# Optimization experiments

Hardware: AMD Instinct MI355X
Metric: run time of the kernel (lower is better)

The kernel has to match this reference:

```python
import jax, jax.numpy as jnp
import numpy as np

D_CONV = 4
DT_RANK = 32
D_STATE = 16


def setup_inputs() -> dict:
    key = jax.random.key(0)
    ks = jax.random.split(key, 12)
    B, Lt, d_model, d_inner = 2, 512, 512, 1024
    mk = lambda k, shape, scale=0.02: jax.random.normal(k, shape, dtype=jnp.float32) * scale
    inp = {}
    inp['t0'] = jax.random.normal(ks[0], (B, Lt, d_model), dtype=jnp.float32)
    inp['t1'] = jax.random.normal(ks[1], (B, Lt, d_model), dtype=jnp.float32)
    inp['t2'] = jax.random.normal(ks[2], (B, Lt, d_model), dtype=jnp.float32)
    inp['t3'] = jax.random.normal(ks[3], (B, Lt, d_model), dtype=jnp.float32)
    inp['in_proj_w'] = mk(ks[4], (2 * d_inner, d_model))
    inp['conv_w'] = mk(ks[5], (d_inner, 1, D_CONV), 0.2)
    inp['conv_b'] = jnp.zeros((d_inner,), jnp.float32)
    inp['x_proj_w'] = mk(ks[6], (DT_RANK + 2 * D_STATE, d_inner))
    s = DT_RANK ** (-0.5)
    inp['dt_w'] = jax.random.uniform(ks[7], (d_inner, DT_RANK), minval=-s, maxval=s, dtype=jnp.float32)
    dt = jnp.exp(jax.random.uniform(ks[8], (d_inner,), dtype=jnp.float32) * (np.log(0.1) - np.log(0.001)) + np.log(0.001))
    dt = jnp.clip(dt, 1e-4)
    inp['dt_b'] = dt + jnp.log(-jnp.expm1(-dt))
    inp['A_log'] = jnp.log(jnp.tile(jnp.arange(1, D_STATE + 1, dtype=jnp.float32), (d_inner, 1)))
    inp['D_param'] = jnp.ones((d_inner,), jnp.float32)
    inp['out_proj_w'] = mk(ks[9], (d_model, d_inner))
    return inp


def reference(t0, t1, t2, t3, in_proj_w, conv_w, conv_b, x_proj_w, dt_w, dt_b, A_log, D_param, out_proj_w):
    tensors = [t0, t1, t2, t3]
    # interleaved gather/concat: [B, 4*Lt, d_model]
    x = jnp.concatenate([t[:, i::4, :] for i in range(4) for t in tensors], axis=1)
    L = x.shape[1]
    xz = x @ in_proj_w.T                      # [B, L, 2*d_inner]
    xc, z = jnp.split(xz, 2, axis=-1)
    # causal depthwise conv1d (torch pads both sides K-1 then truncates to L == left pad only)
    xc = xc.transpose(0, 2, 1)                # [B, d_inner, L]
    xc = jax.lax.conv_general_dilated(
        xc, conv_w, window_strides=(1,), padding=[(D_CONV - 1, 0)],
        dimension_numbers=('NCH', 'OIH', 'NCH'), feature_group_count=xc.shape[1])
    xc = xc + conv_b[None, :, None]
    xc = jax.nn.silu(xc.transpose(0, 2, 1))   # [B, L, d_inner]
    # SSM
    A = -jnp.exp(A_log)                       # [d_inner, d_state]
    dbc = xc @ x_proj_w.T                     # [B, L, dt_rank + 2*d_state]
    delta, Bm, Cm = jnp.split(dbc, [DT_RANK, DT_RANK + D_STATE], axis=-1)
    delta = jax.nn.softplus(delta @ dt_w.T + dt_b)  # [B, L, d_inner]
    deltaA = jnp.exp(delta[..., None] * A)          # [B, L, d_inner, d_state]
    BX = (delta * xc)[..., None] * Bm[:, :, None, :]  # deltaB * x

    def op(c1, c2):
        a1, b1 = c1
        a2, b2 = c2
        return a1 * a2, a2 * b1 + b2

    _, hs = jax.lax.associative_scan(op, (deltaA, BX), axis=1)  # h_t = dA_t h_{t-1} + BX_t
    y = jnp.einsum('blds,bls->bld', hs, Cm) + D_param * xc
    out = (y * jax.nn.silu(z)) @ out_proj_w.T  # [B, L, d_model]
    Lt = L // 4
    return tuple(out[:, i::4, :][:, :Lt, :] + tensors[i] for i in range(4))
```

## Files before the change

kernel.cpp:

```cpp
#include <hip/hip_runtime.h>

#define NB 2
#define LT 512
#define LL 2048
#define MM 4096
#define DMODEL 512
#define DINNER 1024
#define DTRANK 32
#define DSTATE 16
#define NSEG 128
#define SEGLEN 16
#define NST (NB * DINNER * DSTATE)
#define NSCAN (NSEG * NB * DINNER)
#define KCH 8

typedef short bf16x8 __attribute__((ext_vector_type(8)));
typedef float f32x4  __attribute__((ext_vector_type(4)));

__device__ __forceinline__ float silu_f(float x) { return x / (1.f + __expf(-x)); }
__device__ __forceinline__ unsigned short f2b(float f) {
    unsigned u = __float_as_uint(f);
    u += 0x7fffu + ((u >> 16) & 1u);
    return (unsigned short)(u >> 16);
}
__device__ __forceinline__ float b2f(unsigned short u) {
    return __uint_as_float(((unsigned)u) << 16);
}
__device__ __forceinline__ float bhi(unsigned u) {
    return __uint_as_float(u & 0xFFFF0000u);
}
__device__ __forceinline__ float blo(unsigned u) {
    return __uint_as_float(u << 16);
}

__global__ __launch_bounds__(256) void k_prep(
    const float* __restrict__ t0, const float* __restrict__ t1,
    const float* __restrict__ t2, const float* __restrict__ t3,
    const float* __restrict__ Wi, const float* __restrict__ Wx,
    unsigned short* __restrict__ xg_b, unsigned short* __restrict__ wib,
    unsigned short* __restrict__ wxb)
{
    const int blk = blockIdx.x;
    if (blk < 1024) {
        const int idx = blk * 256 + threadIdx.x;
        const int m = idx >> 6;
        const int c8 = (idx & 63) * 8;
        const int b = m >> 11;
        const int l = m & 2047;
        const int c = l >> 7, r = l & 127;
        const int ti = c & 3, ci = c >> 2;
        const float* tp = (ti == 0) ? t0 : (ti == 1) ? t1 : (ti == 2) ? t2 : t3;
        const float* src = tp + ((size_t)b * 512 + (size_t)(ci + 4 * r)) * 512 + c8;
        float4 v0 = *(const float4*)(src + 0);
        float4 v1 = *(const float4*)(src + 4);
        bf16x8 o;
        o[0]=f2b(v0.x); o[1]=f2b(v0.y); o[2]=f2b(v0.z); o[3]=f2b(v0.w);
        o[4]=f2b(v1.x); o[5]=f2b(v1.y); o[6]=f2b(v1.z); o[7]=f2b(v1.w);
        *(bf16x8*)(xg_b + (size_t)m * DMODEL + c8) = o;
    } else if (blk < 2048) {
        const int off = (blk - 1024) * 256 + threadIdx.x;
        float4 v = *(const float4*)(Wi + (size_t)off * 4);
        ushort4 o;
        o.x = f2b(v.x); o.y = f2b(v.y); o.z = f2b(v.z); o.w = f2b(v.w);
        *(ushort4*)(wib + (size_t)off * 4) = o;
    } else {
        const int off = (blk - 2048) * 256 + threadIdx.x;
        float4 v = *(const float4*)(Wx + (size_t)off * 4);
        ushort4 o;
        o.x = f2b(v.x); o.y = f2b(v.y); o.z = f2b(v.z); o.w = f2b(v.w);
        *(ushort4*)(wxb + (size_t)off * 4) = o;
    }
}

__global__ __launch_bounds__(256) void k_inproj(
    const unsigned short* __restrict__ xg_b, const unsigned short* __restrict__ wib,
    float* __restrict__ xc_raw, unsigned short* __restrict__ zb)
{
    __shared__ short As[128 * 40];
    __shared__ short Bs[128 * 40];
    const int t = threadIdx.x;
    const int lane = t & 63;
    const int wid = t >> 6;
    const int wm = wid >> 1, wn = wid & 1;
    const int bm = blockIdx.x, bn = blockIdx.y;

    const int srow  = t >> 1;
    const int shalf = (t & 1) * 16;

    const unsigned short* asrc = xg_b + (size_t)(bm * 128 + srow) * DMODEL + shalf;
    const unsigned short* bsrc = wib + (size_t)(bn * 128 + srow) * DMODEL + shalf;

    f32x4 acc[4][4];
#pragma unroll
    for (int i = 0; i < 4; ++i)
#pragma unroll
        for (int j = 0; j < 4; ++j) acc[i][j] = (f32x4){0.f, 0.f, 0.f, 0.f};

    bf16x8 ra0 = *(const bf16x8*)(asrc + 0);
    bf16x8 ra1 = *(const bf16x8*)(asrc + 8);
    bf16x8 rb0 = *(const bf16x8*)(bsrc + 0);
    bf16x8 rb1 = *(const bf16x8*)(bsrc + 8);

    const int ko = (lane >> 4) * 8;
    const int fr = lane & 15;

    for (int ks = 0; ks < DMODEL / 32; ++ks) {
        __syncthreads();
        *(bf16x8*)&As[srow * 40 + shalf]     = ra0;
        *(bf16x8*)&As[srow * 40 + shalf + 8] = ra1;
        *(bf16x8*)&Bs[srow * 40 + shalf]     = rb0;
        *(bf16x8*)&Bs[srow * 40 + shalf + 8] = rb1;
        __syncthreads();
        if (ks + 1 < DMODEL / 32) {
            const int k0 = (ks + 1) * 32;
            ra0 = *(const bf16x8*)(asrc + k0 + 0);
            ra1 = *(const bf16x8*)(asrc + k0 + 8);
            rb0 = *(const bf16x8*)(bsrc + k0 + 0);
            rb1 = *(const bf16x8*)(bsrc + k0 + 8);
        }
        bf16x8 af[4], bfr[4];
#pragma unroll
        for (int mf = 0; mf < 4; ++mf)
            af[mf] = *(const bf16x8*)&As[(wm * 64 + mf * 16 + fr) * 40 + ko];
#pragma unroll
        for (int nf = 0; nf < 4; ++nf)
            bfr[nf] = *(const bf16x8*)&Bs[(wn * 64 + nf * 16 + fr) * 40 + ko];
#pragma unroll
        for (int mf = 0; mf < 4; ++mf)
#pragma unroll
            for (int nf = 0; nf < 4; ++nf)
                acc[mf][nf] = __builtin_amdgcn_mfma_f32_16x16x32_bf16(
                    af[mf], bfr[nf], acc[mf][nf], 0, 0, 0);
    }

    if (bn < 8) {
#pragma unroll
        for (int mf = 0; mf < 4; ++mf) {
            const int gmb = bm * 128 + wm * 64 + mf * 16 + (lane >> 4) * 4;
#pragma unroll
            for (int nf = 0; nf < 4; ++nf) {
                const int gn = bn * 128 + wn * 64 + nf * 16 + (lane & 15);
#pragma unroll
                for (int j = 0; j < 4; ++j)
                    xc_raw[(size_t)(gmb + j) * DINNER + gn] = acc[mf][nf][j];
            }
        }
    } else {
#pragma unroll
        for (int mf = 0; mf < 4; ++mf) {
            const int gmb = bm * 128 + wm * 64 + mf * 16 + (lane >> 4) * 4;
#pragma unroll
            for (int nf = 0; nf < 4; ++nf) {
                const int gn = bn * 128 + wn * 64 + nf * 16 + (lane & 15) - 1024;
#pragma unroll
                for (int j = 0; j < 4; ++j)
                    zb[(size_t)(gmb + j) * DINNER + gn] = f2b(acc[mf][nf][j]);
            }
        }
    }
}

__global__ __launch_bounds__(256) void k_conv(
    const float* __restrict__ xc_raw, const float* __restrict__ cw,
    const float* __restrict__ cb, const unsigned short* __restrict__ zb,
    unsigned short* __restrict__ xc_b, unsigned int* __restrict__ xzp)
{
    const int d  = blockIdx.y * 256 + threadIdx.x;
    const int mt = blockIdx.x;
    const int m0 = mt * 16;
    const int l0 = m0 & 2047;

    float w[4];
#pragma unroll
    for (int k = 0; k < 4; ++k) w[k] = cw[(size_t)d * 4 + k];
    const float bias = cb[d];

    float r[19];
#pragma unroll
    for (int o = 0; o < 19; ++o) {
        const int l = l0 + o - 3;
        r[o] = (l >= 0) ? xc_raw[(size_t)(m0 + o - 3) * DINNER + d] : 0.f;
    }

#pragma unroll
    for (int mm = 0; mm < 16; ++mm) {
        float s = bias;
#pragma unroll
        for (int k = 0; k < 4; ++k) s += w[k] * r[mm + k];
        const unsigned short x16 = f2b(silu_f(s));
        const size_t idx = (size_t)(m0 + mm) * DINNER + d;
        const unsigned short z16 = zb[idx];
        xc_b[idx] = x16;
        xzp[idx] = ((unsigned)z16 << 16) | (unsigned)x16;
    }
}

__global__ __launch_bounds__(256) void k_xproj_mfma(
    const unsigned short* __restrict__ xc_b, const unsigned short* __restrict__ wxb,
    float* __restrict__ part)
{
    __shared__ short As[128 * 136];
    __shared__ short Bs[64 * 136];
    const int t = threadIdx.x;
    const int lane = t & 63;
    const int w = t >> 6;
    const int bm = blockIdx.x;
    const int kc = blockIdx.y;

    {
        const int row = t >> 1;
        const int cb0 = (t & 1) * 64;
        const unsigned short* src = xc_b + (size_t)(bm * 128 + row) * 1024 + kc * 128 + cb0;
#pragma unroll
        for (int q = 0; q < 8; ++q)
            *(bf16x8*)&As[row * 136 + cb0 + q * 8] = *(const bf16x8*)(src + q * 8);
    }
    {
        const int row = t >> 2;
        const int cb0 = (t & 3) * 32;
        const unsigned short* src = wxb + (size_t)row * 1024 + kc * 128 + cb0;
#pragma unroll
        for (int q = 0; q < 4; ++q)
            *(bf16x8*)&Bs[row * 136 + cb0 + q * 8] = *(const bf16x8*)(src + q * 8);
    }
    __syncthreads();

    const int fr = lane & 15;
    const int ko = (lane >> 4) * 8;

    f32x4 acc[2][4];
#pragma unroll
    for (int i = 0; i < 2; ++i)
#pragma unroll
        for (int j = 0; j < 4; ++j) acc[i][j] = (f32x4){0.f, 0.f, 0.f, 0.f};

#pragma unroll
    for (int ks = 0; ks < 4; ++ks) {
        const int kb = ks * 32 + ko;
        bf16x8 af[2], bfr[4];
#pragma unroll
        for (int mf = 0; mf < 2; ++mf)
            af[mf] = *(const bf16x8*)&As[(w * 32 + mf * 16 + fr) * 136 + kb];
#pragma unroll
        for (int nf = 0; nf < 4; ++nf)
            bfr[nf] = *(const bf16x8*)&Bs[(nf * 16 + fr) * 136 + kb];
#pragma unroll
        for (int mf = 0; mf < 2; ++mf)
#pragma unroll
            for (int nf = 0; nf < 4; ++nf)
                acc[mf][nf] = __builtin_amdgcn_mfma_f32_16x16x32_bf16(
                    af[mf], bfr[nf], acc[mf][nf], 0, 0, 0);
    }

    float* pb = part + (size_t)kc * (MM * 64);
#pragma unroll
    for (int mf = 0; mf < 2; ++mf) {
        const int rb = bm * 128 + w * 32 + mf * 16 + (lane >> 4) * 4;
#pragma unroll
        for (int nf = 0; nf < 4; ++nf) {
            const int col = nf * 16 + (lane & 15);
#pragma unroll
            for (int j = 0; j < 4; ++j)
                pb[(size_t)(rb + j) * 64 + col] = acc[mf][nf][j];
        }
    }
}

__global__ __launch_bounds__(256) void k_xreduce(
    const float* __restrict__ part, float* __restrict__ dbc)
{
    const int i = blockIdx.x * 256 + threadIdx.x;
    float s = 0.f;
#pragma unroll
    for (int kc = 0; kc < KCH; ++kc)
        s += part[(size_t)kc * (MM * 64) + i];
    dbc[i] = s;
}

__global__ __launch_bounds__(256) void k_dtproj(
    const float* __restrict__ dbc, const float* __restrict__ dtw,
    const float* __restrict__ dtb, const unsigned short* __restrict__ xc_b,
    unsigned int* __restrict__ dxp)
{
    const int tid = threadIdx.x;
    const int m0 = blockIdx.x * 16;
    const int d  = blockIdx.y * 256 + tid;

    float w[DTRANK];
#pragma unroll
    for (int q = 0; q < 8; ++q) {
        float4 v = *(const float4*)(dtw + (size_t)d * DTRANK + q * 4);
        w[q * 4 + 0] = v.x; w[q * 4 + 1] = v.y;
        w[q * 4 + 2] = v.z; w[q * 4 + 3] = v.w;
    }
    const float bias = dtb[d];

#pragma unroll 4
    for (int m = 0; m < 16; ++m) {
        const float* bc = dbc + (size_t)(m0 + m) * 64;
        float s0 = bias, s1 = 0.f, s2 = 0.f, s3 = 0.f;
#pragma unroll
        for (int r = 0; r < DTRANK; r += 4) {
            s0 += bc[r + 0] * w[r + 0];
            s1 += bc[r + 1] * w[r + 1];
            s2 += bc[r + 2] * w[r + 2];
            s3 += bc[r + 3] * w[r + 3];
        }
        const float s = (s0 + s1) + (s2 + s3);
        const float sp = (s > 20.f) ? s : __logf(1.f + __expf(s));
        const size_t idx = (size_t)(m0 + m) * DINNER + d;
        const float xv = b2f(xc_b[idx]);
        dxp[idx] = ((unsigned)f2b(sp * xv) << 16) | (unsigned)f2b(sp);
    }
}

__global__ __launch_bounds__(256) void k_scan_partial(
    const unsigned int* __restrict__ dxp, const float* __restrict__ dbc,
    const float* __restrict__ A_log, unsigned int* __restrict__ hab)
{
    __shared__ float Bsh[4][16][16];
    const int gid = blockIdx.x * 256 + threadIdx.x;
    const int d = gid & 1023;
    const int b = (gid >> 10) & (NB - 1);
    const int g = gid >> 11;
    const int w = threadIdx.x >> 6;
    const int lane = threadIdx.x & 63;

    const int mbase = b * LL + g * SEGLEN;

    {
        const int r0 = lane >> 4;
        const int cc = lane & 15;
#pragma unroll
        for (int rq = 0; rq < 4; ++rq) {
            const int row = rq * 4 + r0;
            Bsh[w][row][cc] = dbc[(size_t)(mbase + row) * 64 + 32 + cc];
        }
    }

    float Af[DSTATE];
#pragma unroll
    for (int q = 0; q < 4; ++q) {
        float4 a4 = *(const float4*)(A_log + d * DSTATE + q * 4);
        Af[q * 4 + 0] = -__expf(a4.x);
        Af[q * 4 + 1] = -__expf(a4.y);
        Af[q * 4 + 2] = -__expf(a4.z);
        Af[q * 4 + 3] = -__expf(a4.w);
    }

    unsigned uu[16];
#pragma unroll
    for (int m = 0; m < 16; ++m)
        uu[m] = dxp[(size_t)(mbase + m) * DINNER + d];

    __syncthreads();

    float h[DSTATE], ap[DSTATE];
#pragma unroll
    for (int s = 0; s < DSTATE; ++s) { h[s] = 0.f; ap[s] = 1.f; }

#pragma unroll
    for (int ll = 0; ll < SEGLEN; ++ll) {
        const float de = blo(uu[ll]);
        const float dx = bhi(uu[ll]);
        float Bv[DSTATE];
#pragma unroll
        for (int q = 0; q < 4; ++q)
            *(float4*)&Bv[q * 4] = *(const float4*)&Bsh[w][ll][q * 4];
#pragma unroll
        for (int s = 0; s < DSTATE; ++s) {
            const float dA = __expf(de * Af[s]);
            ap[s] *= dA;
            h[s] = dA * h[s] + dx * Bv[s];
        }
    }

    const size_t base = ((size_t)(b * DINNER + d) * NSEG + g) * 16;
    unsigned ob[16];
#pragma unroll
    for (int s = 0; s < DSTATE; ++s)
        ob[s] = ((unsigned)f2b(h[s]) << 16) | (unsigned)f2b(ap[s]);
#pragma unroll
    for (int q = 0; q < 4; ++q)
        *(uint4*)&hab[base + q * 4] = *(const uint4*)&ob[q * 4];
}

__global__ __launch_bounds__(256) void k_scan_combine(
    const unsigned int* __restrict__ hab, unsigned short* __restrict__ hib)
{
    const int tid = blockIdx.x * 256 + threadIdx.x;
    const int g = tid & 63;
    const size_t bd = (size_t)(tid >> 6);
    const size_t base = (bd * NSEG + 2 * g) * 16;

    unsigned u0[16], u1[16];
#pragma unroll
    for (int q = 0; q < 4; ++q) {
        *(uint4*)&u0[q * 4] = *(const uint4*)&hab[base + q * 4];
        *(uint4*)&u1[q * 4] = *(const uint4*)&hab[base + 16 + q * 4];
    }

    float A0[16], B0[16], A[16], B[16];
#pragma unroll
    for (int s = 0; s < 16; ++s) {
        A0[s] = blo(u0[s]); B0[s] = bhi(u0[s]);
        const float A1 = blo(u1[s]), B1 = bhi(u1[s]);
        A[s] = A1 * A0[s];
        B[s] = A1 * B0[s] + B1;
    }
#pragma unroll
    for (int off = 1; off < 64; off <<= 1) {
#pragma unroll
        for (int s = 0; s < 16; ++s) {
            const float Ap = __shfl_up(A[s], off, 64);
            const float Bp = __shfl_up(B[s], off, 64);
            if (g >= off) { B[s] = A[s] * Bp + B[s]; A[s] = A[s] * Ap; }
        }
    }
    unsigned short E[16], E1[16];
#pragma unroll
    for (int s = 0; s < 16; ++s) {
        float e = __shfl_up(B[s], 1, 64);
        if (g == 0) e = 0.f;
        E[s]  = f2b(e);
        E1[s] = f2b(A0[s] * e + B0[s]);
    }
#pragma unroll
    for (int q = 0; q < 2; ++q) {
        *(bf16x8*)&hib[base + q * 8]      = *(const bf16x8*)&E[q * 8];
        *(bf16x8*)&hib[base + 16 + q * 8] = *(const bf16x8*)&E1[q * 8];
    }
}

__global__ __launch_bounds__(256) void k_scan_final(
    const unsigned int* __restrict__ dxp, const unsigned int* __restrict__ xzp,
    const float* __restrict__ dbc, const float* __restrict__ A_log,
    const float* __restrict__ Dp, const unsigned short* __restrict__ hib,
    unsigned short* __restrict__ yzb)
{
    __shared__ float BC[4][16][32];
    const int gid = blockIdx.x * 256 + threadIdx.x;
    const int d = gid & 1023;
    const int b = (gid >> 10) & (NB - 1);
    const int g = gid >> 11;
    const int w = threadIdx.x >> 6;
    const int lane = threadIdx.x & 63;

    const int mbase = b * LL + g * SEGLEN;

    {
        const int r0 = lane >> 5;
        const int cc = lane & 31;
#pragma unroll
        for (int rq = 0; rq < 8; ++rq) {
            const int row = rq * 2 + r0;
            BC[w][row][cc] = dbc[(size_t)(mbase + row) * 64 + 32 + cc];
        }
    }

    float Af[DSTATE];
#pragma unroll
    for (int q = 0; q < 4; ++q) {
        float4 a4 = *(const float4*)(A_log + d * DSTATE + q * 4);
        Af[q * 4 + 0] = -__expf(a4.x);
        Af[q * 4 + 1] = -__expf(a4.y);
        Af[q * 4 + 2] = -__expf(a4.z);
        Af[q * 4 + 3] = -__expf(a4.w);
    }
    const float Dd = Dp[d];

    unsigned uu[16], vv[16];
#pragma unroll
    for (int m = 0; m < 16; ++m) {
        uu[m] = dxp[(size_t)(mbase + m) * DINNER + d];
        vv[m] = xzp[(size_t)(mbase + m) * DINNER + d];
    }

    float h[DSTATE];
    {
        const size_t base = ((size_t)(b * DINNER + d) * NSEG + g) * 16;
        bf16x8 h0 = *(const bf16x8*)&hib[base];
        bf16x8 h1 = *(const bf16x8*)&hib[base + 8];
#pragma unroll
        for (int s = 0; s < 8; ++s) {
            h[s]     = b2f((unsigned short)h0[s]);
            h[s + 8] = b2f((unsigned short)h1[s]);
        }
    }

    __syncthreads();

#pragma unroll
    for (int ll = 0; ll < SEGLEN; ++ll) {
        const float de = blo(uu[ll]);
        const float dx = bhi(uu[ll]);
        const float x  = blo(vv[ll]);
        const float zz = bhi(vv[ll]);
        float Bv[DSTATE], Cv[DSTATE];
#pragma unroll
        for (int q = 0; q < 4; ++q) {
            *(float4*)&Bv[q * 4] = *(const float4*)&BC[w][ll][q * 4];
            *(float4*)&Cv[q * 4] = *(const float4*)&BC[w][ll][16 + q * 4];
        }
        float y0 = 0.f, y1 = 0.f, y2 = 0.f, y3 = 0.f;
#pragma unroll
        for (int s = 0; s < DSTATE; s += 4) {
            float dA;
            dA = __expf(de * Af[s + 0]); h[s + 0] = dA * h[s + 0] + dx * Bv[s + 0]; y0 += h[s + 0] * Cv[s + 0];
            dA = __expf(de * Af[s + 1]); h[s + 1] = dA * h[s + 1] + dx * Bv[s + 1]; y1 += h[s + 1] * Cv[s + 1];
            dA = __expf(de * Af[s + 2]); h[s + 2] = dA * h[s + 2] + dx * Bv[s + 2]; y2 += h[s + 2] * Cv[s + 2];
            dA = __expf(de * Af[s + 3]); h[s + 3] = dA * h[s + 3] + dx * Bv[s + 3]; y3 += h[s + 3] * Cv[s + 3];
        }
        const float y = (y0 + y1) + (y2 + y3);
        yzb[(size_t)(mbase + ll) * DINNER + d] = f2b((y + Dd * x) * silu_f(zz));
    }
}

__global__ __launch_bounds__(256) void k_outproj(
    const unsigned short* __restrict__ yzb, const float* __restrict__ Wo,
    const float* __restrict__ t0, const float* __restrict__ t1,
    const float* __restrict__ t2, const float* __restrict__ t3,
    float* __restrict__ outp)
{
    __shared__ short As[64 * 40];
    __shared__ short Bs[64 * 40];
    const int t = threadIdx.x;
    const int lane = t & 63;
    const int wid = t >> 6;
    const int wm = wid >> 1, wn = wid & 1;
    const int bm = blockIdx.x;
    const int bn = blockIdx.y;

    const int srow = t >> 2;
    const int scol = (t & 3) * 8;

    const unsigned short* asrc = yzb + (size_t)(bm * 64 + srow) * DINNER + scol;
    const float* bsrc = Wo + (size_t)(bn * 64 + srow) * DINNER + scol;

    f32x4 acc[2][2];
#pragma unroll
    for (int i = 0; i < 2; ++i)
#pragma unroll
        for (int j = 0; j < 2; ++j) acc[i][j] = (f32x4){0.f, 0.f, 0.f, 0.f};

    bf16x8 raA = *(const bf16x8*)asrc;
    float4 rb[2];
#pragma unroll
    for (int q = 0; q < 2; ++q) rb[q] = *(const float4*)(bsrc + q * 4);

    const int ko = (lane >> 4) * 8;
    const int fr = lane & 15;

    for (int ks = 0; ks < DINNER / 32; ++ks) {
        __syncthreads();
        {
            bf16x8 w0;
            w0[0]=f2b(rb[0].x); w0[1]=f2b(rb[0].y); w0[2]=f2b(rb[0].z); w0[3]=f2b(rb[0].w);
            w0[4]=f2b(rb[1].x); w0[5]=f2b(rb[1].y); w0[6]=f2b(rb[1].z); w0[7]=f2b(rb[1].w);
            *(bf16x8*)&As[srow * 40 + scol] = raA;
            *(bf16x8*)&Bs[srow * 40 + scol] = w0;
        }
        __syncthreads();
        if (ks + 1 < DINNER / 32) {
            const int k0 = (ks + 1) * 32;
            raA = *(const bf16x8*)(asrc + k0);
#pragma unroll
            for (int q = 0; q < 2; ++q) rb[q] = *(const float4*)(bsrc + k0 + q * 4);
        }
        bf16x8 af[2], bfr[2];
#pragma unroll
        for (int mf = 0; mf < 2; ++mf)
            af[mf] = *(const bf16x8*)&As[(wm * 32 + mf * 16 + fr) * 40 + ko];
#pragma unroll
        for (int nf = 0; nf < 2; ++nf)
            bfr[nf] = *(const bf16x8*)&Bs[(wn * 32 + nf * 16 + fr) * 40 + ko];
#pragma unroll
        for (int mf = 0; mf < 2; ++mf)
#pragma unroll
            for (int nf = 0; nf < 2; ++nf)
                acc[mf][nf] = __builtin_amdgcn_mfma_f32_16x16x32_bf16(
                    af[mf], bfr[nf], acc[mf][nf], 0, 0, 0);
    }

#pragma unroll
    for (int mf = 0; mf < 2; ++mf) {
#pragma unroll
        for (int j = 0; j < 4; ++j) {
            const int gm = bm * 64 + wm * 32 + mf * 16 + (lane >> 4) * 4 + j;
            const int b = gm >> 11;
            const int l = gm & 2047;
            const int ii = l & 3;
            const int jj = l >> 2;
            const float* tsel = (ii == 0) ? t0 : (ii == 1) ? t1 : (ii == 2) ? t2 : t3;
#pragma unroll
            for (int nf = 0; nf < 2; ++nf) {
                const int gn = bn * 64 + wn * 32 + nf * 16 + (lane & 15);
                const float tv = tsel[((size_t)b * 512 + jj) * 512 + gn];
                outp[(((size_t)ii * NB + b) * 512 + jj) * 512 + gn] = acc[mf][nf][j] + tv;
            }
        }
    }
}

extern "C" void kernel_launch(void* const* d_in, const int* in_sizes, int n_in,
                              void* d_out, int out_size, void* d_ws, size_t ws_size,
                              hipStream_t stream)
{
    const float* t0 = (const float*)d_in[0];
    const float* t1 = (const float*)d_in[1];
    const float* t2 = (const float*)d_in[2];
    const float* t3 = (const float*)d_in[3];
    const float* in_proj_w  = (const float*)d_in[4];
    const float* conv_w     = (const float*)d_in[5];
    const float* conv_b     = (const float*)d_in[6];
    const float* x_proj_w   = (const float*)d_in[7];
    const float* dt_w       = (const float*)d_in[8];
    const float* dt_b       = (const float*)d_in[9];
    const float* A_log      = (const float*)d_in[10];
    const float* D_param    = (const float*)d_in[11];
    const float* out_proj_w = (const float*)d_in[12];
    float* outp = (float*)d_out;

    float* xc_raw = (float*)d_ws;
    unsigned short* xc_b = (unsigned short*)(xc_raw + (size_t)MM * DINNER);
    unsigned int* dxp = (unsigned int*)(xc_b + (size_t)MM * DINNER);
    unsigned int* xzp = dxp + (size_t)MM * DINNER;
    float* dbc  = (float*)(xzp + (size_t)MM * DINNER);
    unsigned int* hab = (unsigned int*)(dbc + (size_t)MM * 64);
    unsigned short* hib = (unsigned short*)(hab + (size_t)NB * DINNER * NSEG * 16);
    float* part  = xc_raw;
    unsigned short* yzb = (unsigned short*)xc_raw;
    unsigned short* zb  = (unsigned short*)hab;
    unsigned short* wxb = hib;
    unsigned short* xg_b = (unsigned short*)dxp;
    unsigned short* wib  = (unsigned short*)xzp;

    k_prep<<<2112, 256, 0, stream>>>(t0, t1, t2, t3, in_proj_w, x_proj_w, xg_b, wib, wxb);
    k_inproj<<<dim3(32, 16), 256, 0, stream>>>(xg_b, wib, xc_raw, zb);
    k_conv<<<dim3(MM / 16, 4), 256, 0, stream>>>(xc_raw, conv_w, conv_b, zb, xc_b, xzp);
    k_xproj_mfma<<<dim3(32, KCH), 256, 0, stream>>>(xc_b, wxb, part);
    k_xreduce<<<(MM * 64) / 256, 256, 0, stream>>>(part, dbc);
    k_dtproj<<<dim3(MM / 16, 4), 256, 0, stream>>>(dbc, dt_w, dt_b, xc_b, dxp);
    k_scan_partial<<<NSCAN / 256, 256, 0, stream>>>(dxp, dbc, A_log, hab);
    k_scan_combine<<<(NB * DINNER * 64) / 256, 256, 0, stream>>>(hab, hib);
    k_scan_final<<<NSCAN / 256, 256, 0, stream>>>(dxp, xzp, dbc, A_log, D_param, hib, yzb);
    k_outproj<<<dim3(64, 8), 256, 0, stream>>>(yzb, out_proj_w, t0, t1, t2, t3, outp);
}
```

Before: 127.6 us.

## Split scan state dimension across four threads per channel

The partial and final scan kernels now assign four threads per (batch, channel, segment), each owning 4 of the 16 SSM states, and launch four times as many threads. In the final scan the per-state output partial sums are combined with two xor shuffles, and only one lane per channel writes. This cuts registers per thread and raises parallelism and occupancy for the latency-bound recurrence. The cost is redundant loads of dxp/xzp per thread, extra shuffles and more blocks.

```diff
diff --git a/kernel.cpp b/kernel.cpp
--- a/kernel.cpp
+++ b/kernel.cpp
@@ -318,34 +318,27 @@
     const unsigned int* __restrict__ dxp, const float* __restrict__ dbc,
     const float* __restrict__ A_log, unsigned int* __restrict__ hab)
 {
-    __shared__ float Bsh[4][16][16];
+    __shared__ float Bsh[16][16];
     const int gid = blockIdx.x * 256 + threadIdx.x;
-    const int d = gid & 1023;
-    const int b = (gid >> 10) & (NB - 1);
-    const int g = gid >> 11;
-    const int w = threadIdx.x >> 6;
-    const int lane = threadIdx.x & 63;
-
+    const int dlocal = gid & 15;
+    const int sg = (gid >> 4) & 3;
+    const int dhi = (gid >> 6) & 63;
+    const int b = (gid >> 12) & (NB - 1);
+    const int g = gid >> 13;
+    const int d = dhi * 16 + dlocal;
     const int mbase = b * LL + g * SEGLEN;
 
     {
-        const int r0 = lane >> 4;
-        const int cc = lane & 15;
-#pragma unroll
-        for (int rq = 0; rq < 4; ++rq) {
-            const int row = rq * 4 + r0;
-            Bsh[w][row][cc] = dbc[(size_t)(mbase + row) * 64 + 32 + cc];
-        }
-    }
-
-    float Af[DSTATE];
-#pragma unroll
-    for (int q = 0; q < 4; ++q) {
-        float4 a4 = *(const float4*)(A_log + d * DSTATE + q * 4);
-        Af[q * 4 + 0] = -__expf(a4.x);
-        Af[q * 4 + 1] = -__expf(a4.y);
-        Af[q * 4 + 2] = -__expf(a4.z);
-        Af[q * 4 + 3] = -__expf(a4.w);
+        const int row = threadIdx.x >> 4;
+        const int cc  = threadIdx.x & 15;
+        Bsh[row][cc] = dbc[(size_t)(mbase + row) * 64 + 32 + cc];
+    }
+
+    float Af[4];
+    {
+        float4 a4 = *(const float4*)(A_log + d * DSTATE + sg * 4);
+        Af[0] = -__expf(a4.x); Af[1] = -__expf(a4.y);
+        Af[2] = -__expf(a4.z); Af[3] = -__expf(a4.w);
     }
 
     unsigned uu[16];
@@ -355,34 +348,27 @@
 
     __syncthreads();
 
-    float h[DSTATE], ap[DSTATE];
-#pragma unroll
-    for (int s = 0; s < DSTATE; ++s) { h[s] = 0.f; ap[s] = 1.f; }
+    float h[4] = {0.f, 0.f, 0.f, 0.f};
+    float ap[4] = {1.f, 1.f, 1.f, 1.f};
 
 #pragma unroll
     for (int ll = 0; ll < SEGLEN; ++ll) {
         const float de = blo(uu[ll]);
         const float dx = bhi(uu[ll]);
-        float Bv[DSTATE];
-#pragma unroll
-        for (int q = 0; q < 4; ++q)
-            *(float4*)&Bv[q * 4] = *(const float4*)&Bsh[w][ll][q * 4];
-#pragma unroll
-        for (int s = 0; s < DSTATE; ++s) {
-            const float dA = __expf(de * Af[s]);
-            ap[s] *= dA;
-            h[s] = dA * h[s] + dx * Bv[s];
-        }
-    }
-
-    const size_t base = ((size_t)(b * DINNER + d) * NSEG + g) * 16;
-    unsigned ob[16];
-#pragma unroll
-    for (int s = 0; s < DSTATE; ++s)
-        ob[s] = ((unsigned)f2b(h[s]) << 16) | (unsigned)f2b(ap[s]);
+        float4 Bv = *(const float4*)&Bsh[ll][sg * 4];
+        float dA;
+        dA = __expf(de * Af[0]); ap[0] *= dA; h[0] = dA * h[0] + dx * Bv.x;
+        dA = __expf(de * Af[1]); ap[1] *= dA; h[1] = dA * h[1] + dx * Bv.y;
+        dA = __expf(de * Af[2]); ap[2] *= dA; h[2] = dA * h[2] + dx * Bv.z;
+        dA = __expf(de * Af[3]); ap[3] *= dA; h[3] = dA * h[3] + dx * Bv.w;
+    }
+
+    const size_t base = ((size_t)(b * DINNER + d) * NSEG + g) * 16 + sg * 4;
+    unsigned ob[4];
 #pragma unroll
     for (int q = 0; q < 4; ++q)
-        *(uint4*)&hab[base + q * 4] = *(const uint4*)&ob[q * 4];
+        ob[q] = ((unsigned)f2b(h[q]) << 16) | (unsigned)f2b(ap[q]);
+    *(uint4*)&hab[base] = *(const uint4*)&ob[0];
 }
 
 __global__ __launch_bounds__(256) void k_scan_combine(
@@ -438,34 +424,30 @@
     const float* __restrict__ Dp, const unsigned short* __restrict__ hib,
     unsigned short* __restrict__ yzb)
 {
-    __shared__ float BC[4][16][32];
+    __shared__ float BC[16][32];
     const int gid = blockIdx.x * 256 + threadIdx.x;
-    const int d = gid & 1023;
-    const int b = (gid >> 10) & (NB - 1);
-    const int g = gid >> 11;
-    const int w = threadIdx.x >> 6;
-    const int lane = threadIdx.x & 63;
-
+    const int dlocal = gid & 15;
+    const int sg = (gid >> 4) & 3;
+    const int dhi = (gid >> 6) & 63;
+    const int b = (gid >> 12) & (NB - 1);
+    const int g = gid >> 13;
+    const int d = dhi * 16 + dlocal;
     const int mbase = b * LL + g * SEGLEN;
 
     {
-        const int r0 = lane >> 5;
-        const int cc = lane & 31;
-#pragma unroll
-        for (int rq = 0; rq < 8; ++rq) {
-            const int row = rq * 2 + r0;
-            BC[w][row][cc] = dbc[(size_t)(mbase + row) * 64 + 32 + cc];
-        }
-    }
-
-    float Af[DSTATE];
-#pragma unroll
-    for (int q = 0; q < 4; ++q) {
-        float4 a4 = *(const float4*)(A_log + d * DSTATE + q * 4);
-        Af[q * 4 + 0] = -__expf(a4.x);
-        Af[q * 4 + 1] = -__expf(a4.y);
-        Af[q * 4 + 2] = -__expf(a4.z);
-        Af[q * 4 + 3] = -__expf(a4.w);
+#pragma unroll
+        for (int q = 0; q < 2; ++q) {
+            const int idx = q * 256 + threadIdx.x;
+            const int row = idx >> 5, cc = idx & 31;
+            BC[row][cc] = dbc[(size_t)(mbase + row) * 64 + 32 + cc];
+        }
+    }
+
+    float Af[4];
+    {
+        float4 a4 = *(const float4*)(A_log + d * DSTATE + sg * 4);
+        Af[0] = -__expf(a4.x); Af[1] = -__expf(a4.y);
+        Af[2] = -__expf(a4.z); Af[3] = -__expf(a4.w);
     }
     const float Dd = Dp[d];
 
@@ -476,16 +458,12 @@
         vv[m] = xzp[(size_t)(mbase + m) * DINNER + d];
     }
 
-    float h[DSTATE];
+    float h[4];
     {
-        const size_t base = ((size_t)(b * DINNER + d) * NSEG + g) * 16;
-        bf16x8 h0 = *(const bf16x8*)&hib[base];
-        bf16x8 h1 = *(const bf16x8*)&hib[base + 8];
-#pragma unroll
-        for (int s = 0; s < 8; ++s) {
-            h[s]     = b2f((unsigned short)h0[s]);
-            h[s + 8] = b2f((unsigned short)h1[s]);
-        }
+        const size_t base = ((size_t)(b * DINNER + d) * NSEG + g) * 16 + sg * 4;
+        ushort4 hv = *(const ushort4*)(hib + base);
+        h[0] = b2f(hv.x); h[1] = b2f(hv.y);
+        h[2] = b2f(hv.z); h[3] = b2f(hv.w);
     }
 
     __syncthreads();
@@ -496,23 +474,18 @@
         const float dx = bhi(uu[ll]);
         const float x  = blo(vv[ll]);
         const float zz = bhi(vv[ll]);
-        float Bv[DSTATE], Cv[DSTATE];
-#pragma unroll
-        for (int q = 0; q < 4; ++q) {
-            *(float4*)&Bv[q * 4] = *(const float4*)&BC[w][ll][q * 4];
-            *(float4*)&Cv[q * 4] = *(const float4*)&BC[w][ll][16 + q * 4];
-        }
-        float y0 = 0.f, y1 = 0.f, y2 = 0.f, y3 = 0.f;
-#pragma unroll
-        for (int s = 0; s < DSTATE; s += 4) {
-            float dA;
-            dA = __expf(de * Af[s + 0]); h[s + 0] = dA * h[s + 0] + dx * Bv[s + 0]; y0 += h[s + 0] * Cv[s + 0];
-            dA = __expf(de * Af[s + 1]); h[s + 1] = dA * h[s + 1] + dx * Bv[s + 1]; y1 += h[s + 1] * Cv[s + 1];
-            dA = __expf(de * Af[s + 2]); h[s + 2] = dA * h[s + 2] + dx * Bv[s + 2]; y2 += h[s + 2] * Cv[s + 2];
-            dA = __expf(de * Af[s + 3]); h[s + 3] = dA * h[s + 3] + dx * Bv[s + 3]; y3 += h[s + 3] * Cv[s + 3];
-        }
-        const float y = (y0 + y1) + (y2 + y3);
-        yzb[(size_t)(mbase + ll) * DINNER + d] = f2b((y + Dd * x) * silu_f(zz));
+        float4 Bv = *(const float4*)&BC[ll][sg * 4];
+        float4 Cv = *(const float4*)&BC[ll][16 + sg * 4];
+        float dA;
+        float yp = 0.f;
+        dA = __expf(de * Af[0]); h[0] = dA * h[0] + dx * Bv.x; yp += h[0] * Cv.x;
+        dA = __expf(de * Af[1]); h[1] = dA * h[1] + dx * Bv.y; yp += h[1] * Cv.y;
+        dA = __expf(de * Af[2]); h[2] = dA * h[2] + dx * Bv.z; yp += h[2] * Cv.z;
+        dA = __expf(de * Af[3]); h[3] = dA * h[3] + dx * Bv.w; yp += h[3] * Cv.w;
+        yp += __shfl_xor(yp, 16, 64);
+        yp += __shfl_xor(yp, 32, 64);
+        if (sg == 0)
+            yzb[(size_t)(mbase + ll) * DINNER + d] = f2b((yp + Dd * x) * silu_f(zz));
     }
 }
 
@@ -641,8 +614,8 @@
     k_xproj_mfma<<<dim3(32, KCH), 256, 0, stream>>>(xc_b, wxb, part);
     k_xreduce<<<(MM * 64) / 256, 256, 0, stream>>>(part, dbc);
     k_dtproj<<<dim3(MM / 16, 4), 256, 0, stream>>>(dbc, dt_w, dt_b, xc_b, dxp);
-    k_scan_partial<<<NSCAN / 256, 256, 0, stream>>>(dxp, dbc, A_log, hab);
+    k_scan_partial<<<(NSCAN * 4) / 256, 256, 0, stream>>>(dxp, dbc, A_log, hab);
     k_scan_combine<<<(NB * DINNER * 64) / 256, 256, 0, stream>>>(hab, hib);
-    k_scan_final<<<NSCAN / 256, 256, 0, stream>>>(dxp, xzp, dbc, A_log, D_param, hib, yzb);
+    k_scan_final<<<(NSCAN * 4) / 256, 256, 0, stream>>>(dxp, xzp, dbc, A_log, D_param, hib, yzb);
     k_outproj<<<dim3(64, 8), 256, 0, stream>>>(yzb, out_proj_w, t0, t1, t2, t3, outp);
 }
```

Measured after the change: 129.3 us. Within noise of the previous version (+1.3%).
